# Optimization experiments

Hardware: AMD Instinct MI355X
Metric: run time of the kernel (lower is better)

The kernel has to match this reference:

```python
import jax, jax.numpy as jnp
import numpy as np

EMBED_DIM = 1024
NUM_HEADS = 16
HEAD_DIM = EMBED_DIM // NUM_HEADS


def setup_inputs() -> dict:
    key = jax.random.key(0)
    k1, k2, k3, k4 = jax.random.split(key, 4)
    B, S, D = 2, 2048, EMBED_DIM
    x = jax.random.normal(k1, (B, S, D), dtype=jnp.float32)
    xpos = jax.random.randint(k2, (B, S), 0, 2048, dtype=jnp.int32)
    # torch nn.Linear weights: [out_features, in_features]; qkv_bias=False -> no qkv bias
    qkv_w = jax.random.normal(k3, (3 * D, D), dtype=jnp.float32) * (D ** -0.5)
    proj_w = jax.random.normal(k4, (D, D), dtype=jnp.float32) * (D ** -0.5)
    proj_b = jnp.zeros((D,), dtype=jnp.float32)
    return {"x": x, "xpos": xpos, "qkv_w": qkv_w, "proj_w": proj_w, "proj_b": proj_b}


def reference(x, xpos, qkv_w, proj_w, proj_b):
    # rope is None, dropout rates are 0, so xpos is unused and dropout is identity.
    B, S, D = x.shape
    H, hd = NUM_HEADS, D // NUM_HEADS
    scale = hd ** -0.5

    qkv = x @ qkv_w.T                                   # [B, S, 3D]
    qkv = qkv.reshape(B, S, 3, H, hd)
    qkv = jnp.transpose(qkv, (0, 3, 2, 1, 4))           # [B, H, 3, S, hd]
    q, k, v = qkv[:, :, 0], qkv[:, :, 1], qkv[:, :, 2]  # each [B, H, S, hd]

    scores = jnp.einsum("bhqd,bhkd->bhqk", q, k) * scale  # [B, H, S, S]
    probs = jax.nn.softmax(scores, axis=-1)
    out = jnp.einsum("bhqk,bhkd->bhqd", probs, v)         # [B, H, S, hd]

    out = jnp.transpose(out, (0, 2, 1, 3)).reshape(B, S, D)
    out = out @ proj_w.T + proj_b
    return out
```

## Files before the change

### kernel.cpp

```cpp
#include <hip/hip_runtime.h>


typedef __bf16 bf16_8 __attribute__((ext_vector_type(8)));
typedef __bf16 bf16_4 __attribute__((ext_vector_type(4)));
typedef __bf16 bf16_2 __attribute__((ext_vector_type(2)));
typedef float floatx4 __attribute__((ext_vector_type(4)));

#define MFMA16 __builtin_amdgcn_mfma_f32_16x16x32_bf16
#define CSCALE 0.1803368801111204f
#define EXP2R  __builtin_amdgcn_exp2f

__device__ __forceinline__ void gld16(const __bf16* g, __bf16* l) {
    __builtin_amdgcn_global_load_lds(
        (const __attribute__((address_space(1))) void*)g,
        (__attribute__((address_space(3))) void*)l, 16, 0, 0);
}

__device__ __forceinline__ unsigned pk_bf16(float a, float b) {
    bf16_2 t;
    t[0] = (__bf16)a; t[1] = (__bf16)b;
    return __builtin_bit_cast(unsigned, t);
}

__global__ __launch_bounds__(256) void cvt_all(
    const float* __restrict__ x, const float* __restrict__ w1,
    const float* __restrict__ w2,
    __bf16* __restrict__ xb, __bf16* __restrict__ w1b, __bf16* __restrict__ w2b)
{
    const int i = blockIdx.x * 256 + threadIdx.x;
    const float* src; __bf16* dst; int off;
    if (i < (1 << 20))                  { src = x;  dst = xb;  off = i; }
    else if (i < (1 << 20) + 786432)    { src = w1; dst = w1b; off = i - (1 << 20); }
    else                                { src = w2; dst = w2b; off = i - (1 << 20) - 786432; }
    float4 v = ((const float4*)src)[off];
    bf16_4 o;
    o[0] = (__bf16)v.x; o[1] = (__bf16)v.y; o[2] = (__bf16)v.z; o[3] = (__bf16)v.w;
    ((bf16_4*)dst)[off] = o;
}

__device__ __forceinline__ void gemm_bt_mainloop(
    const __bf16* __restrict__ A, const __bf16* __restrict__ B,
    int K, __bf16* As, __bf16* Bs, floatx4 (&acc)[4][4])
{
    const int tid  = threadIdx.x;
    const int lane = tid & 63;
    const int wv   = tid >> 6;
    const int quad = lane >> 4;
    const int l15  = lane & 15;
    const int wm   = (wv >> 1) * 64;
    const int wn   = (wv & 1) * 64;

    for (int k0 = 0; k0 < K; k0 += 64) {
        __syncthreads();
#pragma unroll
        for (int it = 0; it < 4; ++it) {
            int cc = it * 256 + tid;
            int row = cc >> 3, kc = cc & 7;
            gld16(A + row * K + k0 + ((kc ^ (row & 7)) * 8), &As[cc * 8]);
        }
#pragma unroll
        for (int it = 0; it < 4; ++it) {
            int cc = it * 256 + tid;
            int row = cc >> 3, kc = cc & 7;
            gld16(B + row * K + k0 + ((kc ^ (row & 7)) * 8), &Bs[cc * 8]);
        }
        __syncthreads();

#pragma unroll
        for (int ks = 0; ks < 2; ++ks) {
            bf16_8 af[4], bf[4];
#pragma unroll
            for (int mt = 0; mt < 4; ++mt) {
                int r = wm + mt * 16 + l15;
                af[mt] = *(const bf16_8*)&As[r * 64 + (((ks * 4 + quad) ^ (r & 7)) * 8)];
            }
#pragma unroll
            for (int nt = 0; nt < 4; ++nt) {
                int r = wn + nt * 16 + l15;
                bf[nt] = *(const bf16_8*)&Bs[r * 64 + (((ks * 4 + quad) ^ (r & 7)) * 8)];
            }
#pragma unroll
            for (int mt = 0; mt < 4; ++mt)
#pragma unroll
                for (int nt = 0; nt < 4; ++nt)
                    acc[mt][nt] = MFMA16(af[mt], bf[nt], acc[mt][nt], 0, 0, 0);
        }
    }
}

__global__ __launch_bounds__(256) void qkv_gemm(
    const __bf16* __restrict__ X, const __bf16* __restrict__ W,
    __bf16* __restrict__ q_ws, __bf16* __restrict__ k_ws, __bf16* __restrict__ vt_ws)
{
    __shared__ __align__(16) __bf16 As[128 * 64];
    __shared__ __align__(16) __bf16 Bs[128 * 64];
    floatx4 acc[4][4] = {};
    const int m0 = blockIdx.y * 128, n0 = blockIdx.x * 128;
    const int c = n0 >> 10;

    const int tid = threadIdx.x, lane = tid & 63, wv = tid >> 6;
    const int quad = lane >> 4, l15 = lane & 15;
    const int wm = (wv >> 1) * 64, wn = (wv & 1) * 64;

    if (c == 2) {
        gemm_bt_mainloop(X + (size_t)m0 * 1024, W + (size_t)n0 * 1024, 1024, As, Bs, acc);
#pragma unroll
        for (int mt = 0; mt < 4; ++mt) {
            const int mbase = m0 + wm + mt * 16 + quad * 4;
            const int b = mbase >> 11, s = mbase & 2047;
#pragma unroll
            for (int nt = 0; nt < 4; ++nt) {
                const int n = n0 + wn + nt * 16 + l15;
                const int h = (n >> 6) & 15, d = n & 63;
                bf16_4 pk;
#pragma unroll
                for (int r = 0; r < 4; ++r) pk[r] = (__bf16)acc[mt][nt][r];
                *(bf16_4*)&vt_ws[((b * 16 + h) * 64 + d) * 2048 + s] = pk;
            }
        }
    } else {
        gemm_bt_mainloop(W + (size_t)n0 * 1024, X + (size_t)m0 * 1024, 1024, As, Bs, acc);
        __bf16* dst = (c == 0) ? q_ws : k_ws;
        const float scale = (c == 1) ? CSCALE : 1.0f;
#pragma unroll
        for (int mt = 0; mt < 4; ++mt) {
            const int nn = n0 + wm + mt * 16 + quad * 4;
            const int h = (nn >> 6) & 15, d0 = nn & 63;
#pragma unroll
            for (int nt = 0; nt < 4; ++nt) {
                const int token = m0 + wn + nt * 16 + l15;
                const int b = token >> 11, s = token & 2047;
                bf16_4 pk;
#pragma unroll
                for (int r = 0; r < 4; ++r) pk[r] = (__bf16)(acc[mt][nt][r] * scale);
                *(bf16_4*)&dst[((b * 16 + h) * 2048 + s) * 64 + d0] = pk;
            }
        }
    }
}

__global__ __launch_bounds__(256) void attn_kernel(
    const __bf16* __restrict__ q_ws, const __bf16* __restrict__ k_ws,
    const __bf16* __restrict__ vt_ws, __bf16* __restrict__ attn_ws)
{
    __shared__ __align__(16) __bf16 Ks [2][64 * 64];
    __shared__ __align__(16) __bf16 Vts[2][64 * 64];
    __shared__ __align__(16) __bf16 Ps [4][2][16][72];

    const int tid = threadIdx.x, lane = tid & 63, w = tid >> 6;
    const int quad = lane >> 4, l15 = lane & 15;
    const int bh = blockIdx.x, qt = blockIdx.y;
    const int q0 = qt * 128;

    const __bf16* qp  = q_ws  + (size_t)bh * (2048 * 64);
    const __bf16* kp  = k_ws  + (size_t)bh * (2048 * 64);
    const __bf16* vtp = vt_ws + (size_t)bh * (64 * 2048);

    const int srow = tid >> 3, skc = tid & 7;
    const int sw   = (skc ^ (srow & 7)) * 8;
    const __bf16* kb0 = kp  + srow * 64 + sw;
    const __bf16* kb1 = kp  + (srow + 32) * 64 + sw;
    const __bf16* vb0 = vtp + srow * 2048 + sw;
    const __bf16* vb1 = vtp + (srow + 32) * 2048 + sw;
    const int ldsoff = (srow * 8 + skc) * 8;

    auto stage = [&](int buf, int ktok) {
        gld16(kb0 + ktok * 64, &Ks[buf][ldsoff]);
        gld16(kb1 + ktok * 64, &Ks[buf][ldsoff + 32 * 8 * 8]);
        gld16(vb0 + ktok,      &Vts[buf][ldsoff]);
        gld16(vb1 + ktok,      &Vts[buf][ldsoff + 32 * 8 * 8]);
    };

    bf16_8 qf[2][2];
#pragma unroll
    for (int qg = 0; qg < 2; ++qg) {
        const int qrow = q0 + w * 32 + qg * 16 + l15;
        qf[qg][0] = *(const bf16_8*)&qp[qrow * 64 + quad * 8];
        qf[qg][1] = *(const bf16_8*)&qp[qrow * 64 + 32 + quad * 8];
    }

    bf16_8 ones;
#pragma unroll
    for (int j = 0; j < 8; ++j) ones[j] = (__bf16)1.0f;

    floatx4 oacc[2][4] = {};
    floatx4 lsum[2] = {};

    auto compute = [&](const __bf16* Kb, const __bf16* Vb) {
        floatx4 sacc[2][4] = {};
#pragma unroll
        for (int ks = 0; ks < 2; ++ks)
#pragma unroll
            for (int kg = 0; kg < 4; ++kg) {
                int krow = kg * 16 + l15;
                bf16_8 kf = *(const bf16_8*)&Kb[krow * 64 + (((ks * 4 + quad) ^ (krow & 7)) * 8)];
                sacc[0][kg] = MFMA16(kf, qf[0][ks], sacc[0][kg], 0, 0, 0);
                sacc[1][kg] = MFMA16(kf, qf[1][ks], sacc[1][kg], 0, 0, 0);
            }

#pragma unroll
        for (int qg = 0; qg < 2; ++qg)
#pragma unroll
            for (int kg = 0; kg < 4; ++kg) {
                uint2 pk;
                pk.x = pk_bf16(EXP2R(sacc[qg][kg][0]), EXP2R(sacc[qg][kg][1]));
                pk.y = pk_bf16(EXP2R(sacc[qg][kg][2]), EXP2R(sacc[qg][kg][3]));
                *(uint2*)&Ps[w][qg][l15][kg * 16 + quad * 4] = pk;
            }
        __asm__ __volatile__("s_waitcnt lgkmcnt(0)" ::: "memory");

#pragma unroll
        for (int ks = 0; ks < 2; ++ks) {
            bf16_8 pf0 = *(const bf16_8*)&Ps[w][0][l15][ks * 32 + quad * 8];
            bf16_8 pf1 = *(const bf16_8*)&Ps[w][1][l15][ks * 32 + quad * 8];
            lsum[0] = MFMA16(ones, pf0, lsum[0], 0, 0, 0);
            lsum[1] = MFMA16(ones, pf1, lsum[1], 0, 0, 0);
#pragma unroll
            for (int dg = 0; dg < 4; ++dg) {
                int drow = dg * 16 + l15;
                bf16_8 vf = *(const bf16_8*)&Vb[drow * 64 + (((ks * 4 + quad) ^ (drow & 7)) * 8)];
                oacc[0][dg] = MFMA16(vf, pf0, oacc[0][dg], 0, 0, 0);
                oacc[1][dg] = MFMA16(vf, pf1, oacc[1][dg], 0, 0, 0);
            }
        }
    };

    stage(0, 0);

#pragma unroll 1
    for (int kt2 = 0; kt2 < 16; ++kt2) {
        const int ktok = kt2 * 128;
        __syncthreads();
        stage(1, ktok + 64);
        compute(Ks[0], Vts[0]);
        __syncthreads();
        if (kt2 + 1 < 16) stage(0, ktok + 128);
        compute(Ks[1], Vts[1]);
    }

    const int b = bh >> 4, h = bh & 15;
#pragma unroll
    for (int qg = 0; qg < 2; ++qg) {
        const float inv_l = 1.0f / lsum[qg][0];
        const int token = b * 2048 + q0 + w * 32 + qg * 16 + l15;
#pragma unroll
        for (int dg = 0; dg < 4; ++dg) {
            bf16_4 ok;
#pragma unroll
            for (int r = 0; r < 4; ++r) ok[r] = (__bf16)(oacc[qg][dg][r] * inv_l);
            *(bf16_4*)&attn_ws[(size_t)token * 1024 + h * 64 + dg * 16 + quad * 4] = ok;
        }
    }
}

__global__ __launch_bounds__(256) void proj_gemm(
    const __bf16* __restrict__ Ain, const __bf16* __restrict__ W,
    const float* __restrict__ bias, float* __restrict__ out)
{
    __shared__ __align__(16) __bf16 As[128 * 64];
    __shared__ __align__(16) __bf16 Bs[64 * 64];
    floatx4 acc[4][2] = {};
    const int m0 = blockIdx.y * 128, n0 = blockIdx.x * 64;

    const int tid = threadIdx.x, lane = tid & 63, wv = tid >> 6;
    const int quad = lane >> 4, l15 = lane & 15;
    const int wm = (wv >> 1) * 64, wn = (wv & 1) * 32;

    const __bf16* A  = Ain + (size_t)m0 * 1024;
    const __bf16* Bp = W   + (size_t)n0 * 1024;

    for (int k0 = 0; k0 < 1024; k0 += 64) {
        __syncthreads();
#pragma unroll
        for (int it = 0; it < 4; ++it) {
            int cc = it * 256 + tid;
            int row = cc >> 3, kc = cc & 7;
            gld16(A + row * 1024 + k0 + ((kc ^ (row & 7)) * 8), &As[cc * 8]);
        }
#pragma unroll
        for (int it = 0; it < 2; ++it) {
            int cc = it * 256 + tid;
            int row = cc >> 3, kc = cc & 7;
            gld16(Bp + row * 1024 + k0 + ((kc ^ (row & 7)) * 8), &Bs[cc * 8]);
        }
        __syncthreads();

#pragma unroll
        for (int ks = 0; ks < 2; ++ks) {
            bf16_8 af[4], bf[2];
#pragma unroll
            for (int mt = 0; mt < 4; ++mt) {
                int r = wm + mt * 16 + l15;
                af[mt] = *(const bf16_8*)&As[r * 64 + (((ks * 4 + quad) ^ (r & 7)) * 8)];
            }
#pragma unroll
            for (int nt = 0; nt < 2; ++nt) {
                int r = wn + nt * 16 + l15;
                bf[nt] = *(const bf16_8*)&Bs[r * 64 + (((ks * 4 + quad) ^ (r & 7)) * 8)];
            }
#pragma unroll
            for (int mt = 0; mt < 4; ++mt)
#pragma unroll
                for (int nt = 0; nt < 2; ++nt)
                    acc[mt][nt] = MFMA16(af[mt], bf[nt], acc[mt][nt], 0, 0, 0);
        }
    }

    float bv[2];
#pragma unroll
    for (int nt = 0; nt < 2; ++nt) bv[nt] = bias[n0 + wn + nt * 16 + l15];

#pragma unroll
    for (int mt = 0; mt < 4; ++mt) {
        const int m = m0 + wm + mt * 16 + quad * 4;
#pragma unroll
        for (int nt = 0; nt < 2; ++nt) {
            const int n = n0 + wn + nt * 16 + l15;
#pragma unroll
            for (int r = 0; r < 4; ++r)
                out[(size_t)(m + r) * 1024 + n] = acc[mt][nt][r] + bv[nt];
        }
    }
}

extern "C" void kernel_launch(void* const* d_in, const int* in_sizes, int n_in,
                              void* d_out, int out_size, void* d_ws, size_t ws_size,
                              hipStream_t stream)
{
    const float* x      = (const float*)d_in[0];
    const float* qkv_w  = (const float*)d_in[2];
    const float* proj_w = (const float*)d_in[3];
    const float* proj_b = (const float*)d_in[4];
    float* out = (float*)d_out;

    const size_t SZ   = 4096 * 1024;
    const size_t WQKV = 3072 * 1024;
    const size_t WPRJ = 1024 * 1024;

    __bf16* xb      = (__bf16*)d_ws;
    __bf16* qkvwb   = xb + SZ;
    __bf16* projwb  = qkvwb + WQKV;
    __bf16* q_ws    = projwb + WPRJ;
    __bf16* k_ws    = q_ws + SZ;
    __bf16* vt_ws   = k_ws + SZ;
    __bf16* attn_ws = vt_ws + SZ;

    cvt_all<<<dim3(8192), 256, 0, stream>>>(x, qkv_w, proj_w, xb, qkvwb, projwb);
    qkv_gemm  <<<dim3(24, 32), 256, 0, stream>>>(xb, qkvwb, q_ws, k_ws, vt_ws);
    attn_kernel<<<dim3(32, 16), 256, 0, stream>>>(q_ws, k_ws, vt_ws, attn_ws);
    proj_gemm <<<dim3(16, 32), 256, 0, stream>>>(attn_ws, projwb, proj_b, out);
}
```

Before: 188.9 us.

## Split attention key range across two half-blocks and merge partial sums

The attention kernel grows to 512 threads: each half of the block handles the same 128 queries over half of the keys (1024 each), and the two halves combine their partial outputs and row sums through LDS at the end. This doubles the waves per block to raise parallelism and hide latency. In exchange it drops the double-buffered prefetch: each key tile is loaded and then waited on by two barriers before compute, which exposes load latency. The merge is valid without a running max because the scores are not max-subtracted, which the code before already relied on.

```diff
diff --git a/kernel.cpp b/kernel.cpp
--- a/kernel.cpp
+++ b/kernel.cpp
@@ -139,42 +139,37 @@
     }
 }
 
-__global__ __launch_bounds__(256) void attn_kernel(
+__global__ __launch_bounds__(512) void attn_kernel(
     const __bf16* __restrict__ q_ws, const __bf16* __restrict__ k_ws,
     const __bf16* __restrict__ vt_ws, __bf16* __restrict__ attn_ws)
 {
     __shared__ __align__(16) __bf16 Ks [2][64 * 64];
     __shared__ __align__(16) __bf16 Vts[2][64 * 64];
-    __shared__ __align__(16) __bf16 Ps [4][2][16][72];
+    __shared__ __align__(16) __bf16 Ps [8][2][16][72];
 
     const int tid = threadIdx.x, lane = tid & 63, w = tid >> 6;
+    const int half = tid >> 8, htid = tid & 255, wh = w & 3;
     const int quad = lane >> 4, l15 = lane & 15;
     const int bh = blockIdx.x, qt = blockIdx.y;
     const int q0 = qt * 128;
+    const int koff = half * 1024;
 
     const __bf16* qp  = q_ws  + (size_t)bh * (2048 * 64);
     const __bf16* kp  = k_ws  + (size_t)bh * (2048 * 64);
     const __bf16* vtp = vt_ws + (size_t)bh * (64 * 2048);
 
-    const int srow = tid >> 3, skc = tid & 7;
+    const int srow = htid >> 3, skc = htid & 7;
     const int sw   = (skc ^ (srow & 7)) * 8;
-    const __bf16* kb0 = kp  + srow * 64 + sw;
-    const __bf16* kb1 = kp  + (srow + 32) * 64 + sw;
-    const __bf16* vb0 = vtp + srow * 2048 + sw;
-    const __bf16* vb1 = vtp + (srow + 32) * 2048 + sw;
+    const __bf16* kb0 = kp  + (size_t)(koff + srow) * 64 + sw;
+    const __bf16* kb1 = kp  + (size_t)(koff + srow + 32) * 64 + sw;
+    const __bf16* vb0 = vtp + (size_t)srow * 2048 + koff + sw;
+    const __bf16* vb1 = vtp + (size_t)(srow + 32) * 2048 + koff + sw;
     const int ldsoff = (srow * 8 + skc) * 8;
 
-    auto stage = [&](int buf, int ktok) {
-        gld16(kb0 + ktok * 64, &Ks[buf][ldsoff]);
-        gld16(kb1 + ktok * 64, &Ks[buf][ldsoff + 32 * 8 * 8]);
-        gld16(vb0 + ktok,      &Vts[buf][ldsoff]);
-        gld16(vb1 + ktok,      &Vts[buf][ldsoff + 32 * 8 * 8]);
-    };
-
     bf16_8 qf[2][2];
 #pragma unroll
     for (int qg = 0; qg < 2; ++qg) {
-        const int qrow = q0 + w * 32 + qg * 16 + l15;
+        const int qrow = q0 + wh * 32 + qg * 16 + l15;
         qf[qg][0] = *(const bf16_8*)&qp[qrow * 64 + quad * 8];
         qf[qg][1] = *(const bf16_8*)&qp[qrow * 64 + 32 + quad * 8];
     }
@@ -186,7 +181,19 @@
     floatx4 oacc[2][4] = {};
     floatx4 lsum[2] = {};
 
-    auto compute = [&](const __bf16* Kb, const __bf16* Vb) {
+#pragma unroll 1
+    for (int kt = 0; kt < 16; ++kt) {
+        const int ko = kt * 64;
+        __syncthreads();
+        gld16(kb0 + ko * 64, &Ks[half][ldsoff]);
+        gld16(kb1 + ko * 64, &Ks[half][ldsoff + 2048]);
+        gld16(vb0 + ko,      &Vts[half][ldsoff]);
+        gld16(vb1 + ko,      &Vts[half][ldsoff + 2048]);
+        __syncthreads();
+
+        const __bf16* Kb = Ks[half];
+        const __bf16* Vb = Vts[half];
+
         floatx4 sacc[2][4] = {};
 #pragma unroll
         for (int ks = 0; ks < 2; ++ks)
@@ -223,32 +230,38 @@
                 oacc[1][dg] = MFMA16(vf, pf1, oacc[1][dg], 0, 0, 0);
             }
         }
-    };
-
-    stage(0, 0);
-
-#pragma unroll 1
-    for (int kt2 = 0; kt2 < 16; ++kt2) {
-        const int ktok = kt2 * 128;
-        __syncthreads();
-        stage(1, ktok + 64);
-        compute(Ks[0], Vts[0]);
-        __syncthreads();
-        if (kt2 + 1 < 16) stage(0, ktok + 128);
-        compute(Ks[1], Vts[1]);
-    }
-
-    const int b = bh >> 4, h = bh & 15;
-#pragma unroll
-    for (int qg = 0; qg < 2; ++qg) {
-        const float inv_l = 1.0f / lsum[qg][0];
-        const int token = b * 2048 + q0 + w * 32 + qg * 16 + l15;
-#pragma unroll
-        for (int dg = 0; dg < 4; ++dg) {
-            bf16_4 ok;
-#pragma unroll
-            for (int r = 0; r < 4; ++r) ok[r] = (__bf16)(oacc[qg][dg][r] * inv_l);
-            *(bf16_4*)&attn_ws[(size_t)token * 1024 + h * 64 + dg * 16 + quad * 4] = ok;
+    }
+
+    __syncthreads();
+    float* comb  = (float*)Ps;
+    float* lcomb = comb + 128 * 68;
+    if (half == 1) {
+#pragma unroll
+        for (int qg = 0; qg < 2; ++qg) {
+            const int q = wh * 32 + qg * 16 + l15;
+#pragma unroll
+            for (int dg = 0; dg < 4; ++dg)
+                *(floatx4*)&comb[q * 68 + dg * 16 + quad * 4] = oacc[qg][dg];
+            if (quad == 0) lcomb[q] = lsum[qg][0];
+        }
+    }
+    __syncthreads();
+    if (half == 0) {
+        const int b = bh >> 4, h = bh & 15;
+#pragma unroll
+        for (int qg = 0; qg < 2; ++qg) {
+            const int q = wh * 32 + qg * 16 + l15;
+            const float inv_l = 1.0f / (lsum[qg][0] + lcomb[q]);
+            const int token = b * 2048 + q0 + q;
+#pragma unroll
+            for (int dg = 0; dg < 4; ++dg) {
+                floatx4 v2 = *(const floatx4*)&comb[q * 68 + dg * 16 + quad * 4];
+                bf16_4 ok;
+#pragma unroll
+                for (int r = 0; r < 4; ++r)
+                    ok[r] = (__bf16)((oacc[qg][dg][r] + v2[r]) * inv_l);
+                *(bf16_4*)&attn_ws[(size_t)token * 1024 + h * 64 + dg * 16 + quad * 4] = ok;
+            }
         }
     }
 }
@@ -347,6 +360,6 @@
 
     cvt_all<<<dim3(8192), 256, 0, stream>>>(x, qkv_w, proj_w, xb, qkvwb, projwb);
     qkv_gemm  <<<dim3(24, 32), 256, 0, stream>>>(xb, qkvwb, q_ws, k_ws, vt_ws);
-    attn_kernel<<<dim3(32, 16), 256, 0, stream>>>(q_ws, k_ws, vt_ws, attn_ws);
+    attn_kernel<<<dim3(32, 16), 512, 0, stream>>>(q_ws, k_ws, vt_ws, attn_ws);
     proj_gemm <<<dim3(16, 32), 256, 0, stream>>>(attn_ws, projwb, proj_b, out);
 }
```

After: 184.1 us. 1.03x faster.
